# Optimization experiments

Measured on AMD Instinct MI355X. Metric: run time of the kernel, lower is better.

## Reference

```python
import jax, jax.numpy as jnp
import numpy as np

N_NODES = 50000
N_EDGES = 800000
IN_CH = 128
HID = 32
HEADS = 4
OUT_CH = 16
NEG_SLOPE = 0.2  # PyG GATConv default LeakyReLU slope


def setup_inputs() -> dict:
    key = jax.random.key(0)
    ks = jax.random.split(key, 12)
    x = jax.random.normal(ks[0], (N_NODES, IN_CH), dtype=jnp.float32)
    edge_index = jax.random.randint(ks[1], (2, N_EDGES), 0, N_NODES, dtype=jnp.int32)
    edge_attr = jax.random.uniform(ks[2], (N_EDGES,), dtype=jnp.float32)
    s = 0.1
    W1 = jax.random.normal(ks[3], (IN_CH, HEADS * HID), dtype=jnp.float32) * s
    a_src1 = jax.random.normal(ks[4], (HEADS, HID), dtype=jnp.float32) * s
    a_dst1 = jax.random.normal(ks[5], (HEADS, HID), dtype=jnp.float32) * s
    b1 = jnp.zeros((HEADS * HID,), dtype=jnp.float32)
    W2 = jax.random.normal(ks[6], (HEADS * HID, OUT_CH), dtype=jnp.float32) * s
    a_src2 = jax.random.normal(ks[7], (1, OUT_CH), dtype=jnp.float32) * s
    a_dst2 = jax.random.normal(ks[8], (1, OUT_CH), dtype=jnp.float32) * s
    b2 = jnp.zeros((OUT_CH,), dtype=jnp.float32)
    return {"x": x, "edge_index": edge_index, "edge_attr": edge_attr,
            "W1": W1, "a_src1": a_src1, "a_dst1": a_dst1, "b1": b1,
            "W2": W2, "a_src2": a_src2, "a_dst2": a_dst2, "b2": b2}


def gat_conv(x, src, dst, num_nodes, W, a_src, a_dst, bias, concat):
    H, C = a_src.shape
    h = (x @ W).reshape(-1, H, C)              # [N,H,C]
    al_src = jnp.sum(h * a_src, axis=-1)       # [N,H]
    al_dst = jnp.sum(h * a_dst, axis=-1)       # [N,H]
    e = jax.nn.leaky_relu(al_src[src] + al_dst[dst], NEG_SLOPE)  # [E,H]
    # segment softmax over incoming edges of each destination node
    m = jax.ops.segment_max(e, dst, num_segments=num_nodes)
    ex = jnp.exp(e - m[dst])
    denom = jax.ops.segment_sum(ex, dst, num_segments=num_nodes)
    alpha = ex / (denom[dst] + 1e-16)          # [E,H]
    out = jax.ops.segment_sum(h[src] * alpha[..., None], dst, num_segments=num_nodes)  # [N,H,C]
    out = out.reshape(num_nodes, H * C) if concat else out.mean(axis=1)
    return out + bias


def reference(x, edge_index, edge_attr, W1, a_src1, a_dst1, b1, W2, a_src2, a_dst2, b2):
    # edge_attr is ignored by GATConv when edge_dim is None (PyG default)
    N = x.shape[0]
    loop = jnp.arange(N, dtype=edge_index.dtype)  # PyG add_self_loops=True
    src = jnp.concatenate([edge_index[0], loop])
    dst = jnp.concatenate([edge_index[1], loop])
    h = jax.nn.elu(gat_conv(x, src, dst, N, W1, a_src1, a_dst1, b1, True))
    out = gat_conv(h, src, dst, N, W2, a_src2, a_dst2, b2, False)
    return jax.nn.log_softmax(out, axis=1)
```

## Files before the change

### kernel.cpp

```cpp
#include <hip/hip_runtime.h>

#define N_NODESC 50000
#define E0C      800000
#define E_TOTC   850000
#define IN_CHC   128
#define HCC      128
#define HEADSC   4
#define OUT_CHC  16
#define NEG_SLOPE 0.2f
#define G1M      64
#define NBUCK    196
#define BNODES   256
#define SBLK     128
#define CHUNK    6656

typedef __attribute__((ext_vector_type(8))) short bf16x8;
typedef __attribute__((ext_vector_type(4))) float f32x4;

__device__ __forceinline__ float lrelu(float v){ return v > 0.f ? v : NEG_SLOPE * v; }

__device__ __forceinline__ unsigned int f2bf(float f){
  unsigned int b = __float_as_uint(f);
  return (b + 0x7fffu + ((b >> 16) & 1u)) >> 16;
}
__device__ __forceinline__ float bf2f(unsigned int lo16){
  return __uint_as_float(lo16 << 16);
}

__global__ void __launch_bounds__(256) k_gemm1(const float* __restrict__ x, const float* __restrict__ W1,
        const float* __restrict__ a_s, const float* __restrict__ a_d,
        unsigned int* __restrict__ h1b, float* __restrict__ al_s, float* __restrict__ al_d)
{
  __shared__ __align__(16) unsigned short Wt[IN_CHC*HCC];
  __shared__ __align__(16) unsigned short xt[G1M*IN_CHC];
  int tid = threadIdx.x, lane = tid & 63, wave = tid >> 6;
  int row0 = blockIdx.x * G1M;

  for (int n0 = 0; n0 < 128; n0 += 64){
    int n = n0 + wave*16 + (lane & 15);
    for (int kc = 0; kc < 128; kc += 32){
      int k = kc + (lane >> 4)*8;
      unsigned int u[4];
      #pragma unroll
      for (int j = 0; j < 8; j += 2){
        float a = W1[(size_t)(k+j)*HCC + n];
        float b = W1[(size_t)(k+j+1)*HCC + n];
        u[j>>1] = f2bf(a) | (f2bf(b) << 16);
      }
      int idx = (n*128 + k) ^ ((n & 7) << 3);
      *(uint4*)&Wt[idx] = make_uint4(u[0],u[1],u[2],u[3]);
    }
  }
  {
    int r  = tid >> 2;
    int kc = (tid & 3) * 32;
    int rr = row0 + r; if (rr > N_NODESC-1) rr = N_NODESC-1;
    const float* xp = &x[(size_t)rr*IN_CHC + kc];
    #pragma unroll
    for (int j = 0; j < 32; j += 8){
      unsigned int u0 = f2bf(xp[j+0]) | (f2bf(xp[j+1]) << 16);
      unsigned int u1 = f2bf(xp[j+2]) | (f2bf(xp[j+3]) << 16);
      unsigned int u2 = f2bf(xp[j+4]) | (f2bf(xp[j+5]) << 16);
      unsigned int u3 = f2bf(xp[j+6]) | (f2bf(xp[j+7]) << 16);
      int idx = (r*128 + kc + j) ^ ((r & 7) << 3);
      *(uint4*)&xt[idx] = make_uint4(u0,u1,u2,u3);
    }
  }
  __syncthreads();

  int rw = wave * 16;
  f32x4 acc[8];
  #pragma unroll
  for (int t = 0; t < 8; t++) acc[t] = (f32x4){0.f,0.f,0.f,0.f};
  #pragma unroll
  for (int kk = 0; kk < 128; kk += 32){
    int m  = rw + (lane & 15);
    int ks = kk + (lane >> 4)*8;
    bf16x8 afrag = *(bf16x8*)&xt[(m*128 + ks) ^ ((m & 7) << 3)];
    #pragma unroll
    for (int t = 0; t < 8; t++){
      int n = t*16 + (lane & 15);
      bf16x8 bfrag = *(bf16x8*)&Wt[(n*128 + ks) ^ ((n & 7) << 3)];
      acc[t] = __builtin_amdgcn_mfma_f32_16x16x32_bf16(afrag, bfrag, acc[t], 0, 0, 0);
    }
  }

  float asv[8], adv[8];
  #pragma unroll
  for (int t = 0; t < 8; t++){
    asv[t] = a_s[t*16 + (lane & 15)];
    adv[t] = a_d[t*16 + (lane & 15)];
  }
  #pragma unroll
  for (int r = 0; r < 4; r++){
    int row = row0 + rw + (lane >> 4)*4 + r;
    bool ok = (row < N_NODESC);
    #pragma unroll
    for (int t = 0; t < 8; t++){
      float v = acc[t][r];
      float o = __shfl_xor(v, 1, 64);
      int c = t*16 + (lane & 15);
      if (ok && ((c & 1) == 0))
        h1b[(size_t)row*64 + (c >> 1)] = f2bf(v) | (f2bf(o) << 16);
    }
    #pragma unroll
    for (int h = 0; h < 4; h++){
      float ps = acc[2*h][r]*asv[2*h] + acc[2*h+1][r]*asv[2*h+1];
      float pd = acc[2*h][r]*adv[2*h] + acc[2*h+1][r]*adv[2*h+1];
      #pragma unroll
      for (int m = 1; m < 16; m <<= 1){ ps += __shfl_xor(ps, m, 64); pd += __shfl_xor(pd, m, 64); }
      if (ok && (lane & 15) == 0){
        al_s[row*HEADSC + h] = ps;
        al_d[row*HEADSC + h] = pd;
      }
    }
  }
}

__global__ void __launch_bounds__(256) k_binA(const int* __restrict__ ei, int* __restrict__ bh){
  __shared__ int h[NBUCK];
  int tid = threadIdx.x, b = blockIdx.x;
  for (int i = tid; i < NBUCK; i += 256) h[i] = 0;
  __syncthreads();
  int e0 = b*CHUNK, e1 = e0 + CHUNK; if (e1 > E_TOTC) e1 = E_TOTC;
  for (int e = e0 + tid; e < e1; e += 256){
    int d = (e < E0C) ? ei[E0C + e] : (e - E0C);
    atomicAdd(&h[d >> 8], 1);
  }
  __syncthreads();
  for (int i = tid; i < NBUCK; i += 256) bh[b*NBUCK + i] = h[i];
}

__global__ void __launch_bounds__(256) k_binscan(int* __restrict__ bh, int* __restrict__ bstart){
  __shared__ int buf[256];
  int tid = threadIdx.x;
  int tot = 0;
  if (tid < NBUCK)
    for (int b = 0; b < SBLK; b++) tot += bh[b*NBUCK + tid];
  buf[tid] = (tid < NBUCK) ? tot : 0;
  __syncthreads();
  #pragma unroll
  for (int off = 1; off < 256; off <<= 1){
    int t = (tid >= off) ? buf[tid - off] : 0;
    __syncthreads();
    buf[tid] += t; __syncthreads();
  }
  int excl = buf[tid] - ((tid < NBUCK) ? tot : 0);
  if (tid < NBUCK) bstart[tid] = excl;
  if (tid == 0) bstart[NBUCK] = E_TOTC;
  __syncthreads();
  if (tid < NBUCK){
    int run = excl;
    for (int b = 0; b < SBLK; b++){
      int t = bh[b*NBUCK + tid];
      bh[b*NBUCK + tid] = run;
      run += t;
    }
  }
}

__global__ void __launch_bounds__(256) k_binB(const int* __restrict__ ei, const int* __restrict__ bh,
                                              unsigned int* __restrict__ binbuf){
  __shared__ int h[NBUCK];
  int tid = threadIdx.x, b = blockIdx.x;
  for (int i = tid; i < NBUCK; i += 256) h[i] = bh[b*NBUCK + i];
  __syncthreads();
  int e0 = b*CHUNK, e1 = e0 + CHUNK; if (e1 > E_TOTC) e1 = E_TOTC;
  for (int e = e0 + tid; e < e1; e += 256){
    int s, d;
    if (e < E0C){ d = ei[E0C + e]; s = ei[e]; }
    else { s = e - E0C; d = s; }
    int pos = atomicAdd(&h[d >> 8], 1);
    binbuf[pos] = ((unsigned int)d << 16) | (unsigned int)s;
  }
}

__global__ void __launch_bounds__(256) k_binC(const unsigned int* __restrict__ binbuf,
                                              const int* __restrict__ bstart,
                                              int* __restrict__ rp, int* __restrict__ srcs){
  __shared__ int lcnt[BNODES];
  __shared__ int buf[BNODES];
  __shared__ int pfx[BNODES];
  int tid = threadIdx.x, k = blockIdx.x;
  int lo = k * BNODES;
  int b0 = bstart[k], b1 = bstart[k+1];
  lcnt[tid] = 0;
  __syncthreads();
  for (int i = b0 + tid; i < b1; i += 256){
    int d = binbuf[i] >> 16;
    atomicAdd(&lcnt[d - lo], 1);
  }
  __syncthreads();
  int v = lcnt[tid];
  buf[tid] = v;
  __syncthreads();
  #pragma unroll
  for (int off = 1; off < 256; off <<= 1){
    int t = (tid >= off) ? buf[tid - off] : 0;
    __syncthreads();
    buf[tid] += t; __syncthreads();
  }
  int excl = buf[tid] - v;
  pfx[tid] = excl;
  int node = lo + tid;
  if (node < N_NODESC) rp[node] = b0 + excl;
  if (k == 0 && tid == 0) rp[N_NODESC] = E_TOTC;
  lcnt[tid] = 0;
  __syncthreads();
  for (int i = b0 + tid; i < b1; i += 256){
    unsigned int u = binbuf[i];
    int d = u >> 16;
    int r = atomicAdd(&lcnt[d - lo], 1);
    srcs[b0 + pfx[d - lo] + r] = (int)(u & 0xffffu);
  }
}

__global__ void __launch_bounds__(256) k_node1(const unsigned int* __restrict__ h1b,
        const float* __restrict__ al_s, const float* __restrict__ al_d,
        const int* __restrict__ rp, const int* __restrict__ srcs,
        const float* __restrict__ b1, float* __restrict__ hout)
{
  int wave = threadIdx.x >> 6, lane = threadIdx.x & 63;
  int n = blockIdx.x*4 + wave;
  if (n >= N_NODESC) return;
  int beg = rp[n], end = rp[n+1];
  int h = lane >> 4;
  float adh = al_d[n*4 + h];
  float dsum = 0.f, acc0 = 0.f, acc1 = 0.f;
  #pragma unroll 4
  for (int p = beg; p < end; p++){
    int s = srcs[p];
    float a = __expf(lrelu(al_s[s*4 + h] + adh));
    unsigned int u = h1b[(size_t)s*64 + lane];
    dsum += a;
    acc0 = fmaf(a, bf2f(u & 0xffffu), acc0);
    acc1 = fmaf(a, bf2f(u >> 16), acc1);
  }
  float inv = 1.f / (dsum + 1e-16f);
  int c0 = lane*2;
  float o0 = acc0*inv + b1[c0], o1 = acc1*inv + b1[c0+1];
  o0 = o0 > 0.f ? o0 : __expf(o0) - 1.f;
  o1 = o1 > 0.f ? o1 : __expf(o1) - 1.f;
  *(float2*)&hout[(size_t)n*HCC + c0] = make_float2(o0, o1);
}

__global__ void __launch_bounds__(256) k_gemm2(const float* __restrict__ hin, const float* __restrict__ W2,
        const float* __restrict__ a_s, const float* __restrict__ a_d,
        unsigned int* __restrict__ h2b, float* __restrict__ al_s, float* __restrict__ al_d)
{
  __shared__ __align__(16) float Wl[IN_CHC*OUT_CHC];
  __shared__ __align__(16) float xr[4][4][IN_CHC];
  int tid = threadIdx.x;
  for (int i = tid*4; i < IN_CHC*OUT_CHC; i += 256*4)
    *(float4*)&Wl[i] = *(const float4*)&W2[i];
  __syncthreads();
  int wave = tid >> 6, lane = tid & 63;
  int r = lane >> 4, c = lane & 15;
  int row0 = blockIdx.x*16 + wave*4;
  for (int rr = 0; rr < 4; rr++){
    float2 v = *(const float2*)&hin[(size_t)(row0+rr)*IN_CHC + lane*2];
    *(float2*)&xr[wave][rr][lane*2] = v;
  }
  float acc = 0.f;
  #pragma unroll 8
  for (int k = 0; k < IN_CHC; k++)
    acc = fmaf(xr[wave][r][k], Wl[k*OUT_CHC + c], acc);
  int row = row0 + r;
  float other = __shfl_xor(acc, 1, 64);
  if ((c & 1) == 0)
    h2b[(size_t)row*8 + (c >> 1)] = f2bf(acc) | (f2bf(other) << 16);
  float ps = acc * a_s[c];
  float pd = acc * a_d[c];
  #pragma unroll
  for (int m = 1; m < 16; m <<= 1){ ps += __shfl_xor(ps, m, 64); pd += __shfl_xor(pd, m, 64); }
  if (c == 0){ al_s[row] = ps; al_d[row] = pd; }
}

__global__ void __launch_bounds__(256) k_node2(const unsigned int* __restrict__ h2b,
        const float* __restrict__ al_s, const float* __restrict__ al_d,
        const int* __restrict__ rp, const int* __restrict__ srcs,
        const float* __restrict__ b2, float* __restrict__ out)
{
  int wave = threadIdx.x >> 6, lane = threadIdx.x & 63;
  int n = blockIdx.x*4 + wave;
  if (n >= N_NODESC) return;
  int beg = rp[n], end = rp[n+1];
  float ad = al_d[n];
  int c = lane & 15, jg = lane >> 4;
  unsigned int hi = (c & 1);
  int widx = c >> 1;
  float dsum = 0.f, acc = 0.f;
  #pragma unroll 4
  for (int p = beg + jg; p < end; p += 4){
    int s = srcs[p];
    float a = __expf(lrelu(al_s[s] + ad));
    unsigned int u = h2b[(size_t)s*8 + widx];
    float hv = __uint_as_float(hi ? (u & 0xFFFF0000u) : (u << 16));
    dsum += a;
    acc = fmaf(a, hv, acc);
  }
  dsum += __shfl_xor(dsum, 16, 64);
  dsum += __shfl_xor(dsum, 32, 64);
  acc += __shfl_xor(acc, 16, 64);
  acc += __shfl_xor(acc, 32, 64);
  float inv = 1.f / (dsum + 1e-16f);
  float v = acc*inv + b2[c];
  float mm = v;
  #pragma unroll
  for (int o = 1; o < 16; o <<= 1) mm = fmaxf(mm, __shfl_xor(mm, o, 64));
  float se = __expf(v - mm);
  #pragma unroll
  for (int o = 1; o < 16; o <<= 1) se += __shfl_xor(se, o, 64);
  if (jg == 0) out[n*OUT_CHC + c] = v - mm - __logf(se);
}

extern "C" void kernel_launch(void* const* d_in, const int* in_sizes, int n_in,
                              void* d_out, int out_size, void* d_ws, size_t ws_size,
                              hipStream_t stream)
{
  const float* x   = (const float*)d_in[0];
  const int*   ei  = (const int*)d_in[1];
  const float* W1  = (const float*)d_in[3];
  const float* as1 = (const float*)d_in[4];
  const float* ad1 = (const float*)d_in[5];
  const float* b1  = (const float*)d_in[6];
  const float* W2  = (const float*)d_in[7];
  const float* as2 = (const float*)d_in[8];
  const float* ad2 = (const float*)d_in[9];
  const float* b2  = (const float*)d_in[10];
  float* out = (float*)d_out;

  char* ws = (char*)d_ws;
  size_t off = 0;
  auto alloc = [&](size_t bytes)->void*{
    void* p = ws + off;
    off = (off + bytes + 255) & ~(size_t)255;
    return p;
  };
  unsigned int* h1b = (unsigned int*)alloc((size_t)N_NODESC*64*4);
  float* hout  = (float*)alloc((size_t)N_NODESC*HCC*4);
  float* al_s1 = (float*)alloc((size_t)N_NODESC*HEADSC*4);
  float* al_d1 = (float*)alloc((size_t)N_NODESC*HEADSC*4);
  unsigned int* h2b = (unsigned int*)alloc((size_t)N_NODESC*8*4);
  float* al_s2 = (float*)alloc((size_t)N_NODESC*4);
  float* al_d2 = (float*)alloc((size_t)N_NODESC*4);
  int* rp      = (int*)alloc((size_t)(N_NODESC+1)*4);
  int* srcs    = (int*)alloc((size_t)E_TOTC*4);
  int* bh      = (int*)alloc((size_t)SBLK*NBUCK*4);
  int* bstart  = (int*)alloc((size_t)(NBUCK+1)*4);
  unsigned int* binbuf = (unsigned int*)alloc((size_t)E_TOTC*4);

  k_gemm1<<<(N_NODESC+G1M-1)/G1M, 256, 0, stream>>>(x, W1, as1, ad1, h1b, al_s1, al_d1);
  k_binA<<<SBLK, 256, 0, stream>>>(ei, bh);
  k_binscan<<<1, 256, 0, stream>>>(bh, bstart);
  k_binB<<<SBLK, 256, 0, stream>>>(ei, bh, binbuf);
  k_binC<<<NBUCK, 256, 0, stream>>>(binbuf, bstart, rp, srcs);
  k_node1<<<(N_NODESC+3)/4, 256, 0, stream>>>(h1b, al_s1, al_d1, rp, srcs, b1, hout);
  k_gemm2<<<N_NODESC/16, 256, 0, stream>>>(hout, W2, as2, ad2, h2b, al_s2, al_d2);
  k_node2<<<(N_NODESC+3)/4, 256, 0, stream>>>(h2b, al_s2, al_d2, rp, srcs, b2, out);
}
```

Before: 150.2 us.

## Fuse layer-2 projection into node1 aggregation, merge binning into GEMM launch, shrink srcs

Merges the edge-bucket histogram pass into the first GEMM launch as extra blocks. Fuses the layer-2 linear projection and its attention logits into the layer-1 aggregation kernel, using a wave-wide shuffle reduction, so the fp32 hidden activations are never written to or re-read from global memory. Stores CSR source indices as 16-bit values to halve gather traffic. This removes two launches and a large intermediate buffer, at the cost of 16 six-step shuffle reductions per node and more registers in node1.

```diff
diff --git a/kernel.cpp b/kernel.cpp
--- a/kernel.cpp
+++ b/kernel.cpp
@@ -9,6 +9,7 @@
 #define OUT_CHC  16
 #define NEG_SLOPE 0.2f
 #define G1M      64
+#define NG1      ((N_NODESC + G1M - 1)/G1M)
 #define NBUCK    196
 #define BNODES   256
 #define SBLK     128
@@ -27,15 +28,31 @@
   return __uint_as_float(lo16 << 16);
 }
 
-__global__ void __launch_bounds__(256) k_gemm1(const float* __restrict__ x, const float* __restrict__ W1,
+__global__ void __launch_bounds__(256) k_gemm1A(const float* __restrict__ x, const float* __restrict__ W1,
         const float* __restrict__ a_s, const float* __restrict__ a_d,
-        unsigned int* __restrict__ h1b, float* __restrict__ al_s, float* __restrict__ al_d)
+        unsigned int* __restrict__ h1b, float* __restrict__ al_s, float* __restrict__ al_d,
+        const int* __restrict__ ei, int* __restrict__ bh)
 {
   __shared__ __align__(16) unsigned short Wt[IN_CHC*HCC];
   __shared__ __align__(16) unsigned short xt[G1M*IN_CHC];
+  __shared__ int hh[NBUCK];
   int tid = threadIdx.x, lane = tid & 63, wave = tid >> 6;
+
+  if (blockIdx.x >= NG1){
+    int b = blockIdx.x - NG1;
+    for (int i = tid; i < NBUCK; i += 256) hh[i] = 0;
+    __syncthreads();
+    int e0 = b*CHUNK, e1 = e0 + CHUNK; if (e1 > E_TOTC) e1 = E_TOTC;
+    for (int e = e0 + tid; e < e1; e += 256){
+      int d = (e < E0C) ? ei[E0C + e] : (e - E0C);
+      atomicAdd(&hh[d >> 8], 1);
+    }
+    __syncthreads();
+    for (int i = tid; i < NBUCK; i += 256) bh[b*NBUCK + i] = hh[i];
+    return;
+  }
+
   int row0 = blockIdx.x * G1M;
-
   for (int n0 = 0; n0 < 128; n0 += 64){
     int n = n0 + wave*16 + (lane & 15);
     for (int kc = 0; kc < 128; kc += 32){
@@ -117,20 +134,6 @@
   }
 }
 
-__global__ void __launch_bounds__(256) k_binA(const int* __restrict__ ei, int* __restrict__ bh){
-  __shared__ int h[NBUCK];
-  int tid = threadIdx.x, b = blockIdx.x;
-  for (int i = tid; i < NBUCK; i += 256) h[i] = 0;
-  __syncthreads();
-  int e0 = b*CHUNK, e1 = e0 + CHUNK; if (e1 > E_TOTC) e1 = E_TOTC;
-  for (int e = e0 + tid; e < e1; e += 256){
-    int d = (e < E0C) ? ei[E0C + e] : (e - E0C);
-    atomicAdd(&h[d >> 8], 1);
-  }
-  __syncthreads();
-  for (int i = tid; i < NBUCK; i += 256) bh[b*NBUCK + i] = h[i];
-}
-
 __global__ void __launch_bounds__(256) k_binscan(int* __restrict__ bh, int* __restrict__ bstart){
   __shared__ int buf[256];
   int tid = threadIdx.x;
@@ -177,7 +180,7 @@
 
 __global__ void __launch_bounds__(256) k_binC(const unsigned int* __restrict__ binbuf,
                                               const int* __restrict__ bstart,
-                                              int* __restrict__ rp, int* __restrict__ srcs){
+                                              int* __restrict__ rp, unsigned short* __restrict__ srcs){
   __shared__ int lcnt[BNODES];
   __shared__ int buf[BNODES];
   __shared__ int pfx[BNODES];
@@ -211,18 +214,26 @@
     unsigned int u = binbuf[i];
     int d = u >> 16;
     int r = atomicAdd(&lcnt[d - lo], 1);
-    srcs[b0 + pfx[d - lo] + r] = (int)(u & 0xffffu);
+    srcs[b0 + pfx[d - lo] + r] = (unsigned short)(u & 0xffffu);
   }
 }
 
 __global__ void __launch_bounds__(256) k_node1(const unsigned int* __restrict__ h1b,
         const float* __restrict__ al_s, const float* __restrict__ al_d,
-        const int* __restrict__ rp, const int* __restrict__ srcs,
-        const float* __restrict__ b1, float* __restrict__ hout)
+        const int* __restrict__ rp, const unsigned short* __restrict__ srcs,
+        const float* __restrict__ b1, const float* __restrict__ W2,
+        const float* __restrict__ as2, const float* __restrict__ ad2,
+        unsigned int* __restrict__ h2b, float* __restrict__ al_s2, float* __restrict__ al_d2)
 {
-  int wave = threadIdx.x >> 6, lane = threadIdx.x & 63;
+  __shared__ float W2t[OUT_CHC][IN_CHC];
+  int tid = threadIdx.x;
+  for (int i = tid; i < IN_CHC*OUT_CHC; i += 256){
+    int k = i >> 4, c = i & 15;
+    W2t[c][k] = W2[i];
+  }
+  __syncthreads();
+  int wave = tid >> 6, lane = tid & 63;
   int n = blockIdx.x*4 + wave;
-  if (n >= N_NODESC) return;
   int beg = rp[n], end = rp[n+1];
   int h = lane >> 4;
   float adh = al_d[n*4 + h];
@@ -241,44 +252,30 @@
   float o0 = acc0*inv + b1[c0], o1 = acc1*inv + b1[c0+1];
   o0 = o0 > 0.f ? o0 : __expf(o0) - 1.f;
   o1 = o1 > 0.f ? o1 : __expf(o1) - 1.f;
-  *(float2*)&hout[(size_t)n*HCC + c0] = make_float2(o0, o1);
-}
-
-__global__ void __launch_bounds__(256) k_gemm2(const float* __restrict__ hin, const float* __restrict__ W2,
-        const float* __restrict__ a_s, const float* __restrict__ a_d,
-        unsigned int* __restrict__ h2b, float* __restrict__ al_s, float* __restrict__ al_d)
-{
-  __shared__ __align__(16) float Wl[IN_CHC*OUT_CHC];
-  __shared__ __align__(16) float xr[4][4][IN_CHC];
-  int tid = threadIdx.x;
-  for (int i = tid*4; i < IN_CHC*OUT_CHC; i += 256*4)
-    *(float4*)&Wl[i] = *(const float4*)&W2[i];
-  __syncthreads();
-  int wave = tid >> 6, lane = tid & 63;
-  int r = lane >> 4, c = lane & 15;
-  int row0 = blockIdx.x*16 + wave*4;
-  for (int rr = 0; rr < 4; rr++){
-    float2 v = *(const float2*)&hin[(size_t)(row0+rr)*IN_CHC + lane*2];
-    *(float2*)&xr[wave][rr][lane*2] = v;
-  }
-  float acc = 0.f;
-  #pragma unroll 8
-  for (int k = 0; k < IN_CHC; k++)
-    acc = fmaf(xr[wave][r][k], Wl[k*OUT_CHC + c], acc);
-  int row = row0 + r;
-  float other = __shfl_xor(acc, 1, 64);
-  if ((c & 1) == 0)
-    h2b[(size_t)row*8 + (c >> 1)] = f2bf(acc) | (f2bf(other) << 16);
-  float ps = acc * a_s[c];
-  float pd = acc * a_d[c];
-  #pragma unroll
-  for (int m = 1; m < 16; m <<= 1){ ps += __shfl_xor(ps, m, 64); pd += __shfl_xor(pd, m, 64); }
-  if (c == 0){ al_s[row] = ps; al_d[row] = pd; }
+  float pp[16];
+  #pragma unroll
+  for (int c = 0; c < 16; c++){
+    float2 w = *(const float2*)&W2t[c][c0];
+    pp[c] = o0*w.x + o1*w.y;
+  }
+  #pragma unroll
+  for (int off = 1; off < 64; off <<= 1){
+    #pragma unroll
+    for (int c = 0; c < 16; c++) pp[c] += __shfl_xor(pp[c], off, 64);
+  }
+  if (lane < 8)
+    h2b[(size_t)n*8 + lane] = f2bf(pp[2*lane]) | (f2bf(pp[2*lane+1]) << 16);
+  if (lane == 0){
+    float ps = 0.f, pd = 0.f;
+    #pragma unroll
+    for (int c = 0; c < 16; c++){ ps += pp[c]*as2[c]; pd += pp[c]*ad2[c]; }
+    al_s2[n] = ps; al_d2[n] = pd;
+  }
 }
 
 __global__ void __launch_bounds__(256) k_node2(const unsigned int* __restrict__ h2b,
         const float* __restrict__ al_s, const float* __restrict__ al_d,
-        const int* __restrict__ rp, const int* __restrict__ srcs,
+        const int* __restrict__ rp, const unsigned short* __restrict__ srcs,
         const float* __restrict__ b2, float* __restrict__ out)
 {
   int wave = threadIdx.x >> 6, lane = threadIdx.x & 63;
@@ -338,24 +335,21 @@
     return p;
   };
   unsigned int* h1b = (unsigned int*)alloc((size_t)N_NODESC*64*4);
-  float* hout  = (float*)alloc((size_t)N_NODESC*HCC*4);
   float* al_s1 = (float*)alloc((size_t)N_NODESC*HEADSC*4);
   float* al_d1 = (float*)alloc((size_t)N_NODESC*HEADSC*4);
   unsigned int* h2b = (unsigned int*)alloc((size_t)N_NODESC*8*4);
   float* al_s2 = (float*)alloc((size_t)N_NODESC*4);
   float* al_d2 = (float*)alloc((size_t)N_NODESC*4);
   int* rp      = (int*)alloc((size_t)(N_NODESC+1)*4);
-  int* srcs    = (int*)alloc((size_t)E_TOTC*4);
+  unsigned short* srcs = (unsigned short*)alloc((size_t)E_TOTC*2);
   int* bh      = (int*)alloc((size_t)SBLK*NBUCK*4);
   int* bstart  = (int*)alloc((size_t)(NBUCK+1)*4);
   unsigned int* binbuf = (unsigned int*)alloc((size_t)E_TOTC*4);
 
-  k_gemm1<<<(N_NODESC+G1M-1)/G1M, 256, 0, stream>>>(x, W1, as1, ad1, h1b, al_s1, al_d1);
-  k_binA<<<SBLK, 256, 0, stream>>>(ei, bh);
+  k_gemm1A<<<NG1 + SBLK, 256, 0, stream>>>(x, W1, as1, ad1, h1b, al_s1, al_d1, ei, bh);
   k_binscan<<<1, 256, 0, stream>>>(bh, bstart);
   k_binB<<<SBLK, 256, 0, stream>>>(ei, bh, binbuf);
   k_binC<<<NBUCK, 256, 0, stream>>>(binbuf, bstart, rp, srcs);
-  k_node1<<<(N_NODESC+3)/4, 256, 0, stream>>>(h1b, al_s1, al_d1, rp, srcs, b1, hout);
-  k_gemm2<<<N_NODESC/16, 256, 0, stream>>>(hout, W2, as2, ad2, h2b, al_s2, al_d2);
-  k_node2<<<(N_NODESC+3)/4, 256, 0, stream>>>(h2b, al_s2, al_d2, rp, srcs, b2, out);
-}
+  k_node1<<<N_NODESC/4, 256, 0, stream>>>(h1b, al_s1, al_d1, rp, srcs, b1, W2, as2, ad2, h2b, al_s2, al_d2);
+  k_node2<<<N_NODESC/4, 256, 0, stream>>>(h2b, al_s2, al_d2, rp, srcs, b2, out);
+}
```

Result: slower. 173.3 us (+15.4%).
